# Performance work log

Measured on AMD Instinct MI355X. Metric: run time of the kernel, lower is better.

## Reference

```python
import jax, jax.numpy as jnp
import numpy as np


def _graph_conv(src, dst, x, num_nodes, inv_sqrt_out, inv_sqrt_in):
    # DGL GraphConv, norm='both': h = D_in^{-1/2} A D_out^{-1/2} x
    msg = (x * inv_sqrt_out[:, None])[src]                      # [E, F] gather
    agg = jax.ops.segment_sum(msg, dst, num_segments=num_nodes)  # [N, F] scatter-add
    return agg * inv_sqrt_in[:, None]


def setup_inputs() -> dict:
    key = jax.random.key(0)
    ks = jax.random.split(key, 8)
    N, E, IN, H, C = 4096, 131072, 512, 8192, 16
    return {
        "features": jax.random.normal(ks[0], (N, IN), dtype=jnp.float32),
        "W1": jax.random.normal(ks[1], (IN, H), dtype=jnp.float32) * 0.02,
        "b1": jnp.zeros((H,), dtype=jnp.float32),
        "W2": jax.random.normal(ks[2], (H, N), dtype=jnp.float32) * 0.02,
        "Wl": jax.random.normal(ks[3], (N, C), dtype=jnp.float32) * 0.02,
        "bl": jnp.zeros((C,), dtype=jnp.float32),
        "src": jax.random.randint(ks[4], (E,), 0, N, dtype=jnp.int32),
        "dst": jax.random.randint(ks[5], (E,), 0, N, dtype=jnp.int32),
    }


def reference(features, W1, b1, W2, Wl, bl, src, dst):
    N = features.shape[0]
    ones = jnp.ones(src.shape, dtype=features.dtype)
    deg_out = jnp.clip(jax.ops.segment_sum(ones, src, num_segments=N), 1.0)
    deg_in = jnp.clip(jax.ops.segment_sum(ones, dst, num_segments=N), 1.0)
    inv_sqrt_out = jax.lax.rsqrt(deg_out)
    inv_sqrt_in = jax.lax.rsqrt(deg_in)

    # conv1: project then aggregate (math identical to DGL's ordering)
    x = features @ W1 + b1
    x = _graph_conv(src, dst, x, N, inv_sqrt_out, inv_sqrt_in)   # [N, 2N]
    # dropout: identity in inference mode
    # conv2 (weight passed externally, no bias)
    x = x @ W2
    x = _graph_conv(src, dst, x, N, inv_sqrt_out, inv_sqrt_in)   # [N, N]
    x = jax.nn.relu(x)
    x = x @ Wl + bl                                              # [N, C]
    return jax.nn.softmax(x, axis=1)
```

## Files before the change

kernel.cpp:

```cpp
#include <hip/hip_runtime.h>
#include <cstdint>
#include <cstddef>


using bf8   = __attribute__((ext_vector_type(8))) short;
using s4    = __attribute__((ext_vector_type(4))) short;
using f32x4 = __attribute__((ext_vector_type(4))) float;

static __device__ __forceinline__ unsigned short f2bf(float f) {
    union { float f; uint32_t u; } v; v.f = f;
    uint32_t r = (v.u + 0x7FFFu + ((v.u >> 16) & 1u)) >> 16;
    return (unsigned short)r;
}
static __device__ __forceinline__ float bf2f(unsigned short b) {
    union { uint32_t u; float f; } v; v.u = ((uint32_t)b) << 16;
    return v.f;
}

static __device__ __forceinline__ void gload16(const short* g, short* l) {
    __builtin_amdgcn_global_load_lds(
        (const __attribute__((address_space(1))) unsigned int*)g,
        (__attribute__((address_space(3))) unsigned int*)l,
        16, 0, 0);
}


__global__ void k_zero(float* a, float* b, int* c, int n) {
    int i = blockIdx.x * blockDim.x + threadIdx.x;
    if (i < n) { a[i] = 0.f; b[i] = 0.f; c[i] = 0; }
}

__global__ void k_count(const int* __restrict__ src, const int* __restrict__ dst,
                        float* deg_out, float* deg_in, int E) {
    int e = blockIdx.x * blockDim.x + threadIdx.x;
    if (e < E) {
        atomicAdd(&deg_out[src[e]], 1.f);
        atomicAdd(&deg_in[dst[e]], 1.f);
    }
}

__global__ void k_inv(const float* deg_out, const float* deg_in,
                      float* inv_out, float* inv_in, int n) {
    int i = blockIdx.x * blockDim.x + threadIdx.x;
    if (i < n) {
        inv_out[i] = rsqrtf(fmaxf(deg_out[i], 1.f));
        inv_in[i]  = rsqrtf(fmaxf(deg_in[i], 1.f));
    }
}

__global__ void k_scan(const float* __restrict__ deg_in, int* __restrict__ row_off) {
    __shared__ int part[1024];
    const int t = threadIdx.x;
    int v0 = (int)deg_in[t*4+0], v1 = (int)deg_in[t*4+1],
        v2 = (int)deg_in[t*4+2], v3 = (int)deg_in[t*4+3];
    part[t] = v0 + v1 + v2 + v3;
    __syncthreads();
    for (int off = 1; off < 1024; off <<= 1) {
        int x = (t >= off) ? part[t - off] : 0;
        __syncthreads();
        part[t] += x;
        __syncthreads();
    }
    int run = (t == 0) ? 0 : part[t-1];
    row_off[t*4+0] = run; run += v0;
    row_off[t*4+1] = run; run += v1;
    row_off[t*4+2] = run; run += v2;
    row_off[t*4+3] = run; run += v3;
    if (t == 1023) row_off[4096] = run;
}

__global__ void k_fill(const int* __restrict__ src, const int* __restrict__ dst,
                       const int* __restrict__ row_off, int* cursor,
                       int* __restrict__ esrc, int E) {
    int e = blockIdx.x * blockDim.x + threadIdx.x;
    if (e < E) {
        int d = dst[e];
        int p = atomicAdd(&cursor[d], 1);
        esrc[row_off[d] + p] = src[e];
    }
}

__global__ void k_rowsum(const int* __restrict__ row_off, const int* __restrict__ esrc,
                         const float* __restrict__ inv_out, const float* __restrict__ inv_in,
                         float* __restrict__ rowsum) {
    const int node = blockIdx.x, lane = threadIdx.x;
    const int beg = row_off[node], end = row_off[node + 1];
    float s = 0.f;
    for (int p = beg + lane; p < end; p += 64) s += inv_out[esrc[p]];
    #pragma unroll
    for (int off = 32; off; off >>= 1) s += __shfl_down(s, off, 64);
    if (lane == 0) rowsum[node] = s * inv_in[node];
}

__global__ void k_cvt_scale(const float* __restrict__ in, const float* __restrict__ sc,
                            short* __restrict__ out, int n4, int f4) {
    int i = blockIdx.x * blockDim.x + threadIdx.x;
    if (i < n4) {
        const float s = sc[i / f4];
        float4 v = reinterpret_cast<const float4*>(in)[i];
        s4 o;
        o[0] = (short)f2bf(v.x * s); o[1] = (short)f2bf(v.y * s);
        o[2] = (short)f2bf(v.z * s); o[3] = (short)f2bf(v.w * s);
        reinterpret_cast<s4*>(out)[i] = o;
    }
}

__global__ __launch_bounds__(256)
void k_tr3(const float* __restrict__ in, short* __restrict__ out, int R, int C) {
    __shared__ float tile[64][65];
    const int bc = blockIdx.x * 64, br = blockIdx.y * 64;
    const int t = threadIdx.x;
    const int rr = t >> 4, cq = (t & 15) * 4;
    #pragma unroll
    for (int p = 0; p < 4; ++p) {
        const int r = rr + p * 16;
        float4 v = *reinterpret_cast<const float4*>(&in[(size_t)(br + r) * C + bc + cq]);
        tile[r][cq + 0] = v.x; tile[r][cq + 1] = v.y;
        tile[r][cq + 2] = v.z; tile[r][cq + 3] = v.w;
    }
    __syncthreads();
    const int cc = t >> 4, rq = (t & 15) * 4;
    #pragma unroll
    for (int p = 0; p < 4; ++p) {
        const int c = cc + p * 16;
        s4 o;
        o[0] = (short)f2bf(tile[rq + 0][c]);
        o[1] = (short)f2bf(tile[rq + 1][c]);
        o[2] = (short)f2bf(tile[rq + 2][c]);
        o[3] = (short)f2bf(tile[rq + 3][c]);
        *reinterpret_cast<s4*>(&out[(size_t)(bc + c) * R + br + rq]) = o;
    }
}

template<int EPI>
__global__ __launch_bounds__(512, 2)
void gemm8p(const short* __restrict__ A, const short* __restrict__ Bt,
            short* __restrict__ C,
            const float* __restrict__ bias, const float* __restrict__ rs,
            int M, int N, int K)
{
    constexpr int USZ  = 4096;
    constexpr int BOFF = 4 * USZ;
    constexpr int BUF  = 8 * USZ;
    __shared__ __align__(16) short lds[2 * BUF];
    const int tid  = threadIdx.x;
    const int wid  = tid >> 6, lane = tid & 63;
    const int wm   = wid >> 2;
    const int wn   = wid & 3;
    const int fr   = lane & 15;
    const int kq   = lane >> 4;
    const int nt   = K >> 6;

    const int gx  = gridDim.x;
    const int nwg = gx * gridDim.y;
    int bid = blockIdx.y * gx + blockIdx.x;
    bid = (bid & 7) * (nwg >> 3) + (bid >> 3);
    const int tm = (bid / gx) * 256;
    const int tn = (bid % gx) * 256;

    const int srow = tid >> 3;
    const int scq  = tid & 7;
    const int scs  = scq ^ (srow & 7);
    const short* gA = A  + (size_t)(tm + srow) * K + scs * 8;
    const short* gB = Bt + (size_t)(tn + srow) * K + scs * 8;
    short* const ldst = lds + tid * 8;

    const int cx0 = (0 * 4 + kq) ^ (fr & 7);
    const int cx1 = (1 * 4 + kq) ^ (fr & 7);
    int aoff[8][2], boff[4][2];
    #pragma unroll
    for (int mi = 0; mi < 8; ++mi) {
        const int r = wm * 128 + mi * 16 + fr;
        aoff[mi][0] = r * 64 + cx0 * 8;
        aoff[mi][1] = r * 64 + cx1 * 8;
    }
    #pragma unroll
    for (int n = 0; n < 4; ++n) {
        const int r = wn * 64 + n * 16 + fr;
        boff[n][0] = BOFF + r * 64 + cx0 * 8;
        boff[n][1] = BOFF + r * 64 + cx1 * 8;
    }

    f32x4 acc[8][4];
    #pragma unroll
    for (int mi = 0; mi < 8; ++mi)
        #pragma unroll
        for (int n = 0; n < 4; ++n)
            acc[mi][n] = (f32x4){0.f, 0.f, 0.f, 0.f};

    #pragma unroll
    for (int u = 0; u < 4; ++u) gload16(gA + (size_t)u * 64 * K, ldst + u * USZ);
    #pragma unroll
    for (int v = 0; v < 4; ++v) gload16(gB + (size_t)v * 64 * K, ldst + BOFF + v * USZ);
    #pragma unroll
    for (int u = 0; u < 4; ++u) gload16(gA + (size_t)u * 64 * K + 64, ldst + BUF + u * USZ);
    #pragma unroll
    for (int v = 0; v < 4; ++v) gload16(gB + (size_t)v * 64 * K + 64, ldst + BUF + BOFF + v * USZ);
    asm volatile("s_waitcnt vmcnt(8)" ::: "memory");
    __builtin_amdgcn_sched_barrier(0);
    __builtin_amdgcn_s_barrier();

    for (int t = 0; t < nt; ++t) {
        const int cc = (t & 1) * BUF;
        const bool pf = (t + 2 < nt);
        const size_t kf = (size_t)(t + 2) * 64;

        bf8 a03[4][2], a47[4][2], bg[4][2];

        #pragma unroll
        for (int mi = 0; mi < 4; ++mi)
            #pragma unroll
            for (int s = 0; s < 2; ++s)
                a03[mi][s] = *reinterpret_cast<const bf8*>(lds + cc + aoff[mi][s]);
        #pragma unroll
        for (int n = 0; n < 2; ++n)
            #pragma unroll
            for (int s = 0; s < 2; ++s)
                bg[n][s] = *reinterpret_cast<const bf8*>(lds + cc + boff[n][s]);
        __builtin_amdgcn_s_barrier();
        asm volatile("s_waitcnt lgkmcnt(0)" ::: "memory");
        __builtin_amdgcn_s_setprio(1);
        #pragma unroll
        for (int mi = 0; mi < 4; ++mi)
            #pragma unroll
            for (int n = 0; n < 2; ++n)
                #pragma unroll
                for (int s = 0; s < 2; ++s)
                    acc[mi][n] = __builtin_amdgcn_mfma_f32_16x16x32_bf16(a03[mi][s], bg[n][s], acc[mi][n], 0, 0, 0);
        __builtin_amdgcn_s_setprio(0);
        __builtin_amdgcn_s_barrier();

        #pragma unroll
        for (int n = 2; n < 4; ++n)
            #pragma unroll
            for (int s = 0; s < 2; ++s)
                bg[n][s] = *reinterpret_cast<const bf8*>(lds + cc + boff[n][s]);
        __builtin_amdgcn_s_barrier();
        asm volatile("s_waitcnt lgkmcnt(0)" ::: "memory");
        __builtin_amdgcn_s_setprio(1);
        #pragma unroll
        for (int mi = 0; mi < 4; ++mi)
            #pragma unroll
            for (int n = 2; n < 4; ++n)
                #pragma unroll
                for (int s = 0; s < 2; ++s)
                    acc[mi][n] = __builtin_amdgcn_mfma_f32_16x16x32_bf16(a03[mi][s], bg[n][s], acc[mi][n], 0, 0, 0);
        __builtin_amdgcn_s_setprio(0);
        __builtin_amdgcn_s_barrier();

        #pragma unroll
        for (int mi = 0; mi < 4; ++mi)
            #pragma unroll
            for (int s = 0; s < 2; ++s)
                a47[mi][s] = *reinterpret_cast<const bf8*>(lds + cc + aoff[4 + mi][s]);
        if (pf) {
            #pragma unroll
            for (int v = 0; v < 4; ++v)
                gload16(gB + (size_t)v * 64 * K + kf, ldst + cc + BOFF + v * USZ);
        }
        __builtin_amdgcn_s_barrier();
        asm volatile("s_waitcnt lgkmcnt(0)" ::: "memory");
        __builtin_amdgcn_s_setprio(1);
        #pragma unroll
        for (int mi = 0; mi < 4; ++mi)
            #pragma unroll
            for (int n = 0; n < 2; ++n)
                #pragma unroll
                for (int s = 0; s < 2; ++s)
                    acc[4 + mi][n] = __builtin_amdgcn_mfma_f32_16x16x32_bf16(a47[mi][s], bg[n][s], acc[4 + mi][n], 0, 0, 0);
        __builtin_amdgcn_s_setprio(0);
        __builtin_amdgcn_s_barrier();

        if (pf) {
            #pragma unroll
            for (int u = 0; u < 4; ++u)
                gload16(gA + (size_t)u * 64 * K + kf, ldst + cc + u * USZ);
        }
        __builtin_amdgcn_s_setprio(1);
        #pragma unroll
        for (int mi = 0; mi < 4; ++mi)
            #pragma unroll
            for (int n = 2; n < 4; ++n)
                #pragma unroll
                for (int s = 0; s < 2; ++s)
                    acc[4 + mi][n] = __builtin_amdgcn_mfma_f32_16x16x32_bf16(a47[mi][s], bg[n][s], acc[4 + mi][n], 0, 0, 0);
        __builtin_amdgcn_s_setprio(0);
        if (pf) {
            asm volatile("s_waitcnt vmcnt(8)" ::: "memory");
        } else if (t + 2 == nt) {
            asm volatile("s_waitcnt vmcnt(0)" ::: "memory");
        }
        __builtin_amdgcn_s_barrier();
    }

    const int rb = kq * 4;
    #pragma unroll
    for (int mi = 0; mi < 8; ++mi) {
        #pragma unroll
        for (int n = 0; n < 4; ++n) {
            const int col = tn + wn * 64 + n * 16 + fr;
            const float bcol = (EPI == 1) ? bias[col] : 0.f;
            #pragma unroll
            for (int j = 0; j < 4; ++j) {
                const int row = tm + wm * 128 + mi * 16 + rb + j;
                float v = acc[mi][n][j];
                if (EPI == 1) v += rs[row] * bcol;
                else          v *= rs[row];
                C[(size_t)row * N + col] = (short)f2bf(v);
            }
        }
    }
}

template<int RELU>
__global__ __launch_bounds__(64)
void agg_strip(const short* __restrict__ X, short* __restrict__ Y,
               const int* __restrict__ row_off, const int* __restrict__ esrc,
               const float* __restrict__ inv_in, int F)
{
    const int node = blockIdx.y;
    const int c0 = blockIdx.x * 512 + threadIdx.x * 8;
    float acc[8];
    #pragma unroll
    for (int j = 0; j < 8; ++j) acc[j] = 0.f;

    const int beg = row_off[node], end = row_off[node + 1];
    int p = beg;
    for (; p + 7 < end; p += 8) {
        bf8 x[8];
        #pragma unroll
        for (int u = 0; u < 8; ++u)
            x[u] = *reinterpret_cast<const bf8*>(X + (size_t)esrc[p + u] * F + c0);
        #pragma unroll
        for (int u = 0; u < 8; ++u)
            #pragma unroll
            for (int j = 0; j < 8; ++j)
                acc[j] += bf2f((unsigned short)x[u][j]);
    }
    for (; p < end; ++p) {
        bf8 x0 = *reinterpret_cast<const bf8*>(X + (size_t)esrc[p] * F + c0);
        #pragma unroll
        for (int j = 0; j < 8; ++j) acc[j] += bf2f((unsigned short)x0[j]);
    }
    const float sc = inv_in[node];
    bf8 o;
    #pragma unroll
    for (int j = 0; j < 8; ++j) {
        float v = acc[j] * sc;
        if (RELU) v = fmaxf(v, 0.f);
        o[j] = (short)f2bf(v);
    }
    *reinterpret_cast<bf8*>(Y + (size_t)node * F + c0) = o;
}

__global__ __launch_bounds__(256)
void k_headgemm(const short* __restrict__ H, const float* __restrict__ Wl,
                float* __restrict__ logitsP)
{
    constexpr int RS = 520;
    __shared__ __align__(16) short ldsB[16 * RS];
    const int tid = threadIdx.x;
    const int m0  = blockIdx.x * 256;
    const int k0  = blockIdx.y * 512;
    const int wid = tid >> 6, lane = tid & 63;
    const int fr  = lane & 15;
    const int kq  = lane >> 4;

    {
        const int c = tid & 15, kk = tid >> 4;
        #pragma unroll
        for (int j = 0; j < 32; ++j) {
            const int k = kk * 32 + j;
            ldsB[c * RS + k] = (short)f2bf(Wl[(size_t)(k0 + k) * 16 + c]);
        }
    }
    __syncthreads();

    const int rb0 = m0 + wid * 64;
    f32x4 acc[4];
    #pragma unroll
    for (int mi = 0; mi < 4; ++mi) acc[mi] = (f32x4){0.f, 0.f, 0.f, 0.f};

    #pragma unroll 4
    for (int s = 0; s < 16; ++s) {
        const bf8 b = *reinterpret_cast<const bf8*>(ldsB + fr * RS + s * 32 + kq * 8);
        #pragma unroll
        for (int mi = 0; mi < 4; ++mi) {
            const bf8 a = *reinterpret_cast<const bf8*>(
                H + (size_t)(rb0 + mi * 16 + fr) * 4096 + k0 + s * 32 + kq * 8);
            acc[mi] = __builtin_amdgcn_mfma_f32_16x16x32_bf16(a, b, acc[mi], 0, 0, 0);
        }
    }

    float* outP = logitsP + (size_t)blockIdx.y * 4096 * 16;
    #pragma unroll
    for (int mi = 0; mi < 4; ++mi)
        #pragma unroll
        for (int j = 0; j < 4; ++j)
            outP[(size_t)(rb0 + mi * 16 + kq * 4 + j) * 16 + fr] = acc[mi][j];
}

__global__ __launch_bounds__(64)
void k_soft(const float* __restrict__ logitsP, const float* __restrict__ bl,
            float* __restrict__ out)
{
    const int node = blockIdx.x * 64 + threadIdx.x;
    float l[16];
    #pragma unroll
    for (int c = 0; c < 16; ++c) l[c] = bl[c];
    for (int p = 0; p < 8; ++p) {
        const float4* lp = reinterpret_cast<const float4*>(
            logitsP + ((size_t)p * 4096 + node) * 16);
        #pragma unroll
        for (int q = 0; q < 4; ++q) {
            float4 v = lp[q];
            l[q*4+0] += v.x; l[q*4+1] += v.y; l[q*4+2] += v.z; l[q*4+3] += v.w;
        }
    }
    float mx = l[0];
    #pragma unroll
    for (int c = 1; c < 16; ++c) mx = fmaxf(mx, l[c]);
    float s = 0.f;
    #pragma unroll
    for (int c = 0; c < 16; ++c) { l[c] = expf(l[c] - mx); s += l[c]; }
    const float inv = 1.f / s;
    float4* o = reinterpret_cast<float4*>(out + (size_t)node * 16);
    #pragma unroll
    for (int q = 0; q < 4; ++q)
        o[q] = make_float4(l[q*4+0]*inv, l[q*4+1]*inv, l[q*4+2]*inv, l[q*4+3]*inv);
}


extern "C" void kernel_launch(void* const* d_in, const int* in_sizes, int n_in,
                              void* d_out, int out_size, void* d_ws, size_t ws_size,
                              hipStream_t stream)
{
    const float* features = (const float*)d_in[0];
    const float* W1       = (const float*)d_in[1];
    const float* b1       = (const float*)d_in[2];
    const float* W2       = (const float*)d_in[3];
    const float* Wl       = (const float*)d_in[4];
    const float* bl       = (const float*)d_in[5];
    const int*   src      = (const int*)d_in[6];
    const int*   dst      = (const int*)d_in[7];
    float* out = (float*)d_out;

    const int N = 4096, IN = 512, H = 8192;
    const int E = in_sizes[6];

    char* ws = (char*)d_ws;
    size_t o = 0;
    auto alloc = [&](size_t bytes) -> char* {
        char* p = ws + o;
        o = (o + bytes + 255) & ~(size_t)255;
        return p;
    };
    short* W2t   = (short*)alloc((size_t)N * H * 2);
    short* h1    = (short*)alloc((size_t)N * H * 2);
    short* x2s   = (short*)alloc((size_t)N * N * 2);
    short* featb = (short*)alloc((size_t)N * IN * 2);
    short* aggF  = (short*)alloc((size_t)N * IN * 2);
    short* W1t   = (short*)alloc((size_t)H * IN * 2);
    float* logitsP = (float*)alloc((size_t)8 * N * 16 * 4);
    float* deg_out = (float*)alloc(N * 4);
    float* deg_in  = (float*)alloc(N * 4);
    float* inv_out = (float*)alloc(N * 4);
    float* inv_in  = (float*)alloc(N * 4);
    float* rowsum  = (float*)alloc(N * 4);
    int*   cursor  = (int*)alloc(N * 4);
    int*   row_off = (int*)alloc((N + 1) * 4);
    int*   esrc    = (int*)alloc((size_t)E * 4);
    short* h2 = h1;

    k_zero <<<(N + 255) / 256, 256, 0, stream>>>(deg_out, deg_in, cursor, N);
    k_count<<<(E + 255) / 256, 256, 0, stream>>>(src, dst, deg_out, deg_in, E);
    k_inv  <<<(N + 255) / 256, 256, 0, stream>>>(deg_out, deg_in, inv_out, inv_in, N);
    k_scan <<<1, 1024, 0, stream>>>(deg_in, row_off);
    k_fill <<<(E + 255) / 256, 256, 0, stream>>>(src, dst, row_off, cursor, esrc, E);
    k_rowsum<<<N, 64, 0, stream>>>(row_off, esrc, inv_out, inv_in, rowsum);

    k_cvt_scale<<<(N * IN / 4 + 255) / 256, 256, 0, stream>>>(features, inv_out, featb,
                                                              N * IN / 4, IN / 4);
    k_tr3<<<dim3(H / 64, IN / 64), 256, 0, stream>>>(W1, W1t, IN, H);
    k_tr3<<<dim3(N / 64, H / 64), 256, 0, stream>>>(W2, W2t, H, N);

    agg_strip<0><<<dim3(1, N), 64, 0, stream>>>(featb, aggF, row_off, esrc, inv_in, IN);
    gemm8p<1><<<dim3(H / 256, N / 256), 512, 0, stream>>>(aggF, W1t, h1, b1, rowsum, N, H, IN);

    gemm8p<2><<<dim3(N / 256, N / 256), 512, 0, stream>>>(h1, W2t, x2s, nullptr, inv_out, N, N, H);
    agg_strip<1><<<dim3(N / 512, N), 64, 0, stream>>>(x2s, h2, row_off, esrc, inv_in, N);

    k_headgemm<<<dim3(N / 256, 8), 256, 0, stream>>>(h2, Wl, logitsP);
    k_soft<<<N / 64, 64, 0, stream>>>(logitsP, bl, out);
}
```

Before: 433.1 us.

## Shrink GEMM tiles to 128x128 with 256 threads and simpler double-buffered loop

The bf16 MFMA GEMM moves from 256x256 tiles with 8 waves to 128x128 tiles with 4 waves. The four-phase interleaved main loop, with its priority bumps and staggered prefetches, becomes a simple per-k-step structure: wait on loads, compute all MFMAs, then issue the next prefetch. This gives more workgroups (1024 for the N×N GEMM) and lower LDS and register use. In exchange each tile reuses operands less, global and L2 traffic grows, and there is less overlap of loads with compute.

```diff
diff --git a/kernel.cpp b/kernel.cpp
--- a/kernel.cpp
+++ b/kernel.cpp
@@ -133,20 +133,20 @@
 }
 
 template<int EPI>
-__global__ __launch_bounds__(512, 2)
+__global__ __launch_bounds__(256, 2)
 void gemm8p(const short* __restrict__ A, const short* __restrict__ Bt,
             short* __restrict__ C,
             const float* __restrict__ bias, const float* __restrict__ rs,
             int M, int N, int K)
 {
-    constexpr int USZ  = 4096;
+    constexpr int USZ  = 2048;
     constexpr int BOFF = 4 * USZ;
     constexpr int BUF  = 8 * USZ;
     __shared__ __align__(16) short lds[2 * BUF];
     const int tid  = threadIdx.x;
     const int wid  = tid >> 6, lane = tid & 63;
-    const int wm   = wid >> 2;
-    const int wn   = wid & 3;
+    const int wm   = wid >> 1;
+    const int wn   = wid & 1;
     const int fr   = lane & 15;
     const int kq   = lane >> 4;
     const int nt   = K >> 6;
@@ -155,8 +155,8 @@
     const int nwg = gx * gridDim.y;
     int bid = blockIdx.y * gx + blockIdx.x;
     bid = (bid & 7) * (nwg >> 3) + (bid >> 3);
-    const int tm = (bid / gx) * 256;
-    const int tn = (bid % gx) * 256;
+    const int tm = (bid / gx) * 128;
+    const int tn = (bid % gx) * 128;
 
     const int srow = tid >> 3;
     const int scq  = tid & 7;
@@ -167,10 +167,10 @@
 
     const int cx0 = (0 * 4 + kq) ^ (fr & 7);
     const int cx1 = (1 * 4 + kq) ^ (fr & 7);
-    int aoff[8][2], boff[4][2];
-    #pragma unroll
-    for (int mi = 0; mi < 8; ++mi) {
-        const int r = wm * 128 + mi * 16 + fr;
+    int aoff[4][2], boff[4][2];
+    #pragma unroll
+    for (int mi = 0; mi < 4; ++mi) {
+        const int r = wm * 64 + mi * 16 + fr;
         aoff[mi][0] = r * 64 + cx0 * 8;
         aoff[mi][1] = r * 64 + cx1 * 8;
     }
@@ -181,128 +181,70 @@
         boff[n][1] = BOFF + r * 64 + cx1 * 8;
     }
 
-    f32x4 acc[8][4];
-    #pragma unroll
-    for (int mi = 0; mi < 8; ++mi)
+    f32x4 acc[4][4];
+    #pragma unroll
+    for (int mi = 0; mi < 4; ++mi)
         #pragma unroll
         for (int n = 0; n < 4; ++n)
             acc[mi][n] = (f32x4){0.f, 0.f, 0.f, 0.f};
 
     #pragma unroll
-    for (int u = 0; u < 4; ++u) gload16(gA + (size_t)u * 64 * K, ldst + u * USZ);
-    #pragma unroll
-    for (int v = 0; v < 4; ++v) gload16(gB + (size_t)v * 64 * K, ldst + BOFF + v * USZ);
-    #pragma unroll
-    for (int u = 0; u < 4; ++u) gload16(gA + (size_t)u * 64 * K + 64, ldst + BUF + u * USZ);
-    #pragma unroll
-    for (int v = 0; v < 4; ++v) gload16(gB + (size_t)v * 64 * K + 64, ldst + BUF + BOFF + v * USZ);
-    asm volatile("s_waitcnt vmcnt(8)" ::: "memory");
-    __builtin_amdgcn_sched_barrier(0);
-    __builtin_amdgcn_s_barrier();
+    for (int u = 0; u < 4; ++u) gload16(gA + (size_t)u * 32 * K, ldst + u * USZ);
+    #pragma unroll
+    for (int v = 0; v < 4; ++v) gload16(gB + (size_t)v * 32 * K, ldst + BOFF + v * USZ);
+    #pragma unroll
+    for (int u = 0; u < 4; ++u) gload16(gA + (size_t)u * 32 * K + 64, ldst + BUF + u * USZ);
+    #pragma unroll
+    for (int v = 0; v < 4; ++v) gload16(gB + (size_t)v * 32 * K + 64, ldst + BUF + BOFF + v * USZ);
 
     for (int t = 0; t < nt; ++t) {
         const int cc = (t & 1) * BUF;
-        const bool pf = (t + 2 < nt);
-        const size_t kf = (size_t)(t + 2) * 64;
-
-        bf8 a03[4][2], a47[4][2], bg[4][2];
-
-        #pragma unroll
-        for (int mi = 0; mi < 4; ++mi)
-            #pragma unroll
-            for (int s = 0; s < 2; ++s)
-                a03[mi][s] = *reinterpret_cast<const bf8*>(lds + cc + aoff[mi][s]);
-        #pragma unroll
-        for (int n = 0; n < 2; ++n)
-            #pragma unroll
-            for (int s = 0; s < 2; ++s)
-                bg[n][s] = *reinterpret_cast<const bf8*>(lds + cc + boff[n][s]);
+
+        if (t + 1 < nt) { asm volatile("s_waitcnt vmcnt(8)" ::: "memory"); }
+        else            { asm volatile("s_waitcnt vmcnt(0)" ::: "memory"); }
+        __builtin_amdgcn_sched_barrier(0);
         __builtin_amdgcn_s_barrier();
+
+        #pragma unroll
+        for (int s = 0; s < 2; ++s) {
+            bf8 b[4], a[4];
+            #pragma unroll
+            for (int n = 0; n < 4; ++n)
+                b[n] = *reinterpret_cast<const bf8*>(lds + cc + boff[n][s]);
+            #pragma unroll
+            for (int mi = 0; mi < 4; ++mi)
+                a[mi] = *reinterpret_cast<const bf8*>(lds + cc + aoff[mi][s]);
+            #pragma unroll
+            for (int mi = 0; mi < 4; ++mi)
+                #pragma unroll
+                for (int n = 0; n < 4; ++n)
+                    acc[mi][n] = __builtin_amdgcn_mfma_f32_16x16x32_bf16(a[mi], b[n], acc[mi][n], 0, 0, 0);
+        }
+
         asm volatile("s_waitcnt lgkmcnt(0)" ::: "memory");
-        __builtin_amdgcn_s_setprio(1);
-        #pragma unroll
-        for (int mi = 0; mi < 4; ++mi)
-            #pragma unroll
-            for (int n = 0; n < 2; ++n)
-                #pragma unroll
-                for (int s = 0; s < 2; ++s)
-                    acc[mi][n] = __builtin_amdgcn_mfma_f32_16x16x32_bf16(a03[mi][s], bg[n][s], acc[mi][n], 0, 0, 0);
-        __builtin_amdgcn_s_setprio(0);
+        __builtin_amdgcn_sched_barrier(0);
         __builtin_amdgcn_s_barrier();
-
-        #pragma unroll
-        for (int n = 2; n < 4; ++n)
-            #pragma unroll
-            for (int s = 0; s < 2; ++s)
-                bg[n][s] = *reinterpret_cast<const bf8*>(lds + cc + boff[n][s]);
-        __builtin_amdgcn_s_barrier();
-        asm volatile("s_waitcnt lgkmcnt(0)" ::: "memory");
-        __builtin_amdgcn_s_setprio(1);
-        #pragma unroll
-        for (int mi = 0; mi < 4; ++mi)
-            #pragma unroll
-            for (int n = 2; n < 4; ++n)
-                #pragma unroll
-                for (int s = 0; s < 2; ++s)
-                    acc[mi][n] = __builtin_amdgcn_mfma_f32_16x16x32_bf16(a03[mi][s], bg[n][s], acc[mi][n], 0, 0, 0);
-        __builtin_amdgcn_s_setprio(0);
-        __builtin_amdgcn_s_barrier();
-
-        #pragma unroll
-        for (int mi = 0; mi < 4; ++mi)
-            #pragma unroll
-            for (int s = 0; s < 2; ++s)
-                a47[mi][s] = *reinterpret_cast<const bf8*>(lds + cc + aoff[4 + mi][s]);
-        if (pf) {
+        if (t + 2 < nt) {
+            const size_t kf = (size_t)(t + 2) * 64;
+            #pragma unroll
+            for (int u = 0; u < 4; ++u)
+                gload16(gA + (size_t)u * 32 * K + kf, ldst + cc + u * USZ);
             #pragma unroll
             for (int v = 0; v < 4; ++v)
-                gload16(gB + (size_t)v * 64 * K + kf, ldst + cc + BOFF + v * USZ);
-        }
-        __builtin_amdgcn_s_barrier();
-        asm volatile("s_waitcnt lgkmcnt(0)" ::: "memory");
-        __builtin_amdgcn_s_setprio(1);
-        #pragma unroll
-        for (int mi = 0; mi < 4; ++mi)
-            #pragma unroll
-            for (int n = 0; n < 2; ++n)
-                #pragma unroll
-                for (int s = 0; s < 2; ++s)
-                    acc[4 + mi][n] = __builtin_amdgcn_mfma_f32_16x16x32_bf16(a47[mi][s], bg[n][s], acc[4 + mi][n], 0, 0, 0);
-        __builtin_amdgcn_s_setprio(0);
-        __builtin_amdgcn_s_barrier();
-
-        if (pf) {
-            #pragma unroll
-            for (int u = 0; u < 4; ++u)
-                gload16(gA + (size_t)u * 64 * K + kf, ldst + cc + u * USZ);
-        }
-        __builtin_amdgcn_s_setprio(1);
-        #pragma unroll
-        for (int mi = 0; mi < 4; ++mi)
-            #pragma unroll
-            for (int n = 2; n < 4; ++n)
-                #pragma unroll
-                for (int s = 0; s < 2; ++s)
-                    acc[4 + mi][n] = __builtin_amdgcn_mfma_f32_16x16x32_bf16(a47[mi][s], bg[n][s], acc[4 + mi][n], 0, 0, 0);
-        __builtin_amdgcn_s_setprio(0);
-        if (pf) {
-            asm volatile("s_waitcnt vmcnt(8)" ::: "memory");
-        } else if (t + 2 == nt) {
-            asm volatile("s_waitcnt vmcnt(0)" ::: "memory");
-        }
-        __builtin_amdgcn_s_barrier();
+                gload16(gB + (size_t)v * 32 * K + kf, ldst + cc + BOFF + v * USZ);
+        }
     }
 
     const int rb = kq * 4;
     #pragma unroll
-    for (int mi = 0; mi < 8; ++mi) {
+    for (int mi = 0; mi < 4; ++mi) {
         #pragma unroll
         for (int n = 0; n < 4; ++n) {
             const int col = tn + wn * 64 + n * 16 + fr;
             const float bcol = (EPI == 1) ? bias[col] : 0.f;
             #pragma unroll
             for (int j = 0; j < 4; ++j) {
-                const int row = tm + wm * 128 + mi * 16 + rb + j;
+                const int row = tm + wm * 64 + mi * 16 + rb + j;
                 float v = acc[mi][n][j];
                 if (EPI == 1) v += rs[row] * bcol;
                 else          v *= rs[row];
@@ -485,9 +427,9 @@
     k_tr3<<<dim3(N / 64, H / 64), 256, 0, stream>>>(W2, W2t, H, N);
 
     agg_strip<0><<<dim3(1, N), 64, 0, stream>>>(featb, aggF, row_off, esrc, inv_in, IN);
-    gemm8p<1><<<dim3(H / 256, N / 256), 512, 0, stream>>>(aggF, W1t, h1, b1, rowsum, N, H, IN);
-
-    gemm8p<2><<<dim3(N / 256, N / 256), 512, 0, stream>>>(h1, W2t, x2s, nullptr, inv_out, N, N, H);
+    gemm8p<1><<<dim3(H / 128, N / 128), 256, 0, stream>>>(aggF, W1t, h1, b1, rowsum, N, H, IN);
+
+    gemm8p<2><<<dim3(N / 128, N / 128), 256, 0, stream>>>(h1, W2t, x2s, nullptr, inv_out, N, N, H);
     agg_strip<1><<<dim3(N / 512, N), 64, 0, stream>>>(x2s, h2, row_off, esrc, inv_in, N);
 
     k_headgemm<<<dim3(N / 256, 8), 256, 0, stream>>>(h2, Wl, logitsP);
```

Result: slower. 534.2 us (+23.4%).
